# Kernel tuning notes

Hardware: AMD Instinct MI355X
Metric: run time of the kernel (lower is better)

## Reference

```python
import jax, jax.numpy as jnp
import numpy as np

N = 100000
E = 1600000
IN_C = 128
HID = 64
OUT_C = 112


def setup_inputs() -> dict:
    key = jax.random.key(0)
    ks = jax.random.split(key, 10)
    x = jax.random.normal(ks[0], (N, IN_C), dtype=jnp.float32)
    edge_index = jax.random.randint(ks[1], (2, E), 0, N, dtype=jnp.int32)
    s1 = 1.0 / np.sqrt(IN_C)
    s2 = 1.0 / np.sqrt(HID)
    return {
        "x": x,
        "edge_index": edge_index,
        "W1l": jax.random.uniform(ks[2], (IN_C, HID), jnp.float32, -s1, s1),
        "b1": jnp.zeros((HID,), jnp.float32),
        "W1r": jax.random.uniform(ks[3], (IN_C, HID), jnp.float32, -s1, s1),
        "W2l": jax.random.uniform(ks[4], (HID, HID), jnp.float32, -s2, s2),
        "b2": jnp.zeros((HID,), jnp.float32),
        "W2r": jax.random.uniform(ks[5], (HID, HID), jnp.float32, -s2, s2),
        "Wo": jax.random.uniform(ks[6], (HID, OUT_C), jnp.float32, -s2, s2),
        "bo": jnp.zeros((OUT_C,), jnp.float32),
    }


def _sage_conv(x, src, dst, Wl, b, Wr):
    # mean-aggregate neighbor messages (src -> dst), then linear + root linear
    msg = x[src]                                             # [E, F] gather
    agg = jax.ops.segment_sum(msg, dst, num_segments=N)      # [N, F] scatter-add
    deg = jax.ops.segment_sum(jnp.ones((src.shape[0],), x.dtype), dst, num_segments=N)
    mean = agg / jnp.maximum(deg, 1.0)[:, None]
    return mean @ Wl + b + x @ Wr


def reference(x, edge_index, W1l, b1, W1r, W2l, b2, W2r, Wo, bo):
    src, dst = edge_index[0], edge_index[1]
    h = jax.nn.relu(_sage_conv(x, src, dst, W1l, b1, W1r))
    # dropout disabled (inference / eval mode)
    h = jax.nn.relu(_sage_conv(h, src, dst, W2l, b2, W2r))
    return h @ Wo + bo
```

## Files before the change

### kernel.cpp

```cpp
#include <hip/hip_runtime.h>

typedef float f32x4 __attribute__((ext_vector_type(4)));
typedef short s16x8 __attribute__((ext_vector_type(8)));
typedef short s16x4 __attribute__((ext_vector_type(4)));

__device__ __forceinline__ unsigned short f2bf(float f) {
    unsigned u = __builtin_bit_cast(unsigned, f);
    unsigned r = (u + 0x7FFFu + ((u >> 16) & 1u)) >> 16;
    return (unsigned short)r;
}
__device__ __forceinline__ float bf2f(unsigned short h) {
    unsigned u = ((unsigned)h) << 16;
    return __builtin_bit_cast(float, u);
}
__device__ __forceinline__ float bflo(unsigned u) {
    return __builtin_bit_cast(float, u << 16);
}
__device__ __forceinline__ float bfhi(unsigned u) {
    return __builtin_bit_cast(float, u & 0xffff0000u);
}

__global__ __launch_bounds__(256)
void pack_frags(const float* __restrict__ W1l, const float* __restrict__ W1r,
                const float* __restrict__ W2l, const float* __restrict__ W2r,
                const float* __restrict__ Wo,
                short* __restrict__ PH1, short* __restrict__ PL1,
                short* __restrict__ PH2, short* __restrict__ PL2,
                short* __restrict__ PHo, short* __restrict__ PLo)
{
    const int tot = 2048 + 1024 + 896;
    for (int e = blockIdx.x * 256 + threadIdx.x; e < tot; e += gridDim.x * 256) {
        int lane, f, k0, c, stride;
        const float* W;
        short *PH, *PL;
        int idx;
        if (e < 2048) {
            idx = e; lane = e & 63; f = e >> 6;
            int kt = f & 3, ct = (f >> 2) & 3, m = f >> 4;
            W = m ? W1r : W1l; PH = PH1; PL = PL1;
            k0 = kt * 32 + ((lane >> 4) << 3);
            c  = ct * 16 + (lane & 15);
            stride = 64;
        } else if (e < 3072) {
            int e2 = e - 2048;
            idx = e2; lane = e2 & 63; f = e2 >> 6;
            int kt = f & 1, ct = (f >> 1) & 3, m = f >> 3;
            W = m ? W2r : W2l; PH = PH2; PL = PL2;
            k0 = kt * 32 + ((lane >> 4) << 3);
            c  = ct * 16 + (lane & 15);
            stride = 64;
        } else {
            int eo = e - 3072;
            idx = eo; lane = eo & 63; f = eo >> 6;
            int kt = f & 1, ct = f >> 1;
            W = Wo; PH = PHo; PL = PLo;
            k0 = kt * 32 + ((lane >> 4) << 3);
            c  = ct * 16 + (lane & 15);
            stride = 112;
        }
        short h[8], l[8];
        #pragma unroll
        for (int j = 0; j < 8; ++j) {
            float v = W[(size_t)(k0 + j) * stride + c];
            unsigned short hb = f2bf(v);
            h[j] = (short)hb;
            l[j] = (short)f2bf(v - bf2f(hb));
        }
        #pragma unroll
        for (int j = 0; j < 8; ++j) { PH[idx * 8 + j] = h[j]; PL[idx * 8 + j] = l[j]; }
    }
}

__global__ __launch_bounds__(512)
void fused_gemm1_count(const float* __restrict__ X, const short* __restrict__ PH,
                       const short* __restrict__ PL, unsigned short* __restrict__ Yl,
                       unsigned short* __restrict__ Yr, int n,
                       const int* __restrict__ dst, int* __restrict__ gcount,
                       int E, int B, int gemmBlocks)
{
    __shared__ unsigned short sT[8][16 * 72];
    __shared__ int lh[512];

    if ((int)blockIdx.x >= gemmBlocks) {
        for (int i = threadIdx.x; i < B; i += 512) lh[i] = 0;
        __syncthreads();
        long base = (long)(blockIdx.x - gemmBlocks) * 8192;
        #pragma unroll
        for (int j = 0; j < 16; ++j) {
            long e = base + j * 512 + threadIdx.x;
            if (e < E) atomicAdd(&lh[dst[e] >> 9], 1);
        }
        __syncthreads();
        for (int i = threadIdx.x; i < B; i += 512) {
            int v = lh[i];
            if (v) atomicAdd(&gcount[i], v);
        }
        return;
    }

    constexpr int K = 128, NKT = 4;
    const int lane = threadIdx.x & 63;
    const int wid  = threadIdx.x >> 6;
    const long ntile = ((long)n + 15) >> 4;
    long t = (long)blockIdx.x * 8 + wid;
    if (t >= ntile) return;
    const long rbase = t << 4;
    long arow = rbase + (lane & 15);
    if (arow >= n) arow = n - 1;
    const int koff = (lane >> 4) << 3;
    const float* xr = X + arow * K + koff;

    s16x8 Bh[NKT], Bl[NKT];
    #pragma unroll
    for (int kt = 0; kt < NKT; ++kt) {
        f32x4 a0 = *(const f32x4*)(xr + kt * 32);
        f32x4 a1 = *(const f32x4*)(xr + kt * 32 + 4);
        s16x8 h, l;
        #pragma unroll
        for (int j = 0; j < 4; ++j) {
            float v = a0[j]; unsigned short hb = f2bf(v);
            h[j] = (short)hb; l[j] = (short)f2bf(v - bf2f(hb));
            float v2 = a1[j]; unsigned short hb2 = f2bf(v2);
            h[4 + j] = (short)hb2; l[4 + j] = (short)f2bf(v2 - bf2f(hb2));
        }
        Bh[kt] = h; Bl[kt] = l;
    }

    f32x4 acc[2][4];
    #pragma unroll
    for (int m = 0; m < 2; ++m)
        #pragma unroll
        for (int ct = 0; ct < 4; ++ct) acc[m][ct] = (f32x4)(0.f);

    #pragma unroll
    for (int m = 0; m < 2; ++m)
    #pragma unroll
    for (int ct = 0; ct < 4; ++ct)
    #pragma unroll
    for (int kt = 0; kt < NKT; ++kt) {
        const int fidx = ((((m << 2) | ct) * NKT) + kt) * 64 + lane;
        s16x8 Ah = *(const s16x8*)(PH + (size_t)fidx * 8);
        s16x8 Al = *(const s16x8*)(PL + (size_t)fidx * 8);
        acc[m][ct] = __builtin_amdgcn_mfma_f32_16x16x32_bf16(Ah, Bh[kt], acc[m][ct], 0, 0, 0);
        acc[m][ct] = __builtin_amdgcn_mfma_f32_16x16x32_bf16(Al, Bh[kt], acc[m][ct], 0, 0, 0);
        acc[m][ct] = __builtin_amdgcn_mfma_f32_16x16x32_bf16(Ah, Bl[kt], acc[m][ct], 0, 0, 0);
    }

    const int wrow = lane & 15, q4 = (lane >> 4) << 2;
    #pragma unroll
    for (int m = 0; m < 2; ++m) {
        unsigned short* __restrict__ Y = m ? Yr : Yl;
        #pragma unroll
        for (int ct = 0; ct < 4; ++ct) {
            s16x4 pv;
            #pragma unroll
            for (int j = 0; j < 4; ++j) pv[j] = (short)f2bf(acc[m][ct][j]);
            *(s16x4*)&sT[wid][wrow * 72 + ct * 16 + q4] = pv;
        }
        asm volatile("s_waitcnt lgkmcnt(0)" ::: "memory");
        if (rbase + 16 <= (long)n) {
            #pragma unroll
            for (int s = 0; s < 2; ++s) {
                int f = s * 64 + lane;
                s16x8 v = *(const s16x8*)&sT[wid][(f >> 3) * 72 + ((f & 7) << 3)];
                *(s16x8*)&Y[rbase * 64 + (size_t)f * 8] = v;
            }
        } else {
            #pragma unroll
            for (int s = 0; s < 2; ++s) {
                int f = s * 64 + lane;
                s16x8 v = *(const s16x8*)&sT[wid][(f >> 3) * 72 + ((f & 7) << 3)];
                long g = rbase * 64 + (size_t)f * 8;
                #pragma unroll
                for (int jj = 0; jj < 8; ++jj)
                    if (g + jj < (long)n * 64) Y[g + jj] = (unsigned short)v[jj];
            }
        }
        asm volatile("s_waitcnt lgkmcnt(0)" ::: "memory");
    }
}


__global__ void bucket_scan(const int* __restrict__ gcount, int* __restrict__ gbase,
                            int* __restrict__ gcursor, int B, int E)
{
    __shared__ int s[256];
    int t = threadIdx.x;
    int v = (t < B) ? gcount[t] : 0;
    s[t] = v;
    __syncthreads();
    for (int off = 1; off < 256; off <<= 1) {
        int u = (t >= off) ? s[t - off] : 0;
        __syncthreads();
        s[t] += u;
        __syncthreads();
    }
    int ex = s[t] - v;
    if (t < B) { gbase[t] = ex; gcursor[t] = ex; }
    if (t == 0) gbase[B] = E;
}

__global__ __launch_bounds__(256)
void bucket_scatter(const int* __restrict__ src, const int* __restrict__ dst,
                    int* __restrict__ gcursor, int* __restrict__ packed, int E, int B)
{
    __shared__ int lh[256];
    __shared__ int lbase[256];
    for (int i = threadIdx.x; i < B; i += 256) lh[i] = 0;
    __syncthreads();
    long base = (long)blockIdx.x * 4096;
    int bkt[16], rnk[16], pk[16];
    #pragma unroll
    for (int j = 0; j < 16; ++j) {
        long e = base + j * 256 + threadIdx.x;
        if (e < E) {
            int d = dst[e], s = src[e];
            bkt[j] = d >> 9;
            pk[j]  = (s << 9) | (d & 511);
            rnk[j] = atomicAdd(&lh[bkt[j]], 1);
        } else bkt[j] = -1;
    }
    __syncthreads();
    for (int i = threadIdx.x; i < B; i += 256) {
        int v = lh[i];
        lbase[i] = v ? atomicAdd(&gcursor[i], v) : 0;
    }
    __syncthreads();
    #pragma unroll
    for (int j = 0; j < 16; ++j)
        if (bkt[j] >= 0) packed[lbase[bkt[j]] + rnk[j]] = pk[j];
}

__global__ __launch_bounds__(256)
void bucket_hist(const int* __restrict__ packed, const int* __restrict__ gbase,
                 int* __restrict__ degi, int n)
{
    __shared__ int h[512];
    int b = blockIdx.x, nb = b << 9;
    int cnt = n - nb; if (cnt > 512) cnt = 512;
    for (int i = threadIdx.x; i < 512; i += 256) h[i] = 0;
    __syncthreads();
    int s = gbase[b], e = gbase[b + 1];
    for (int i = s + threadIdx.x; i < e; i += 256)
        atomicAdd(&h[packed[i] & 511], 1);
    __syncthreads();
    for (int i = threadIdx.x; i < cnt; i += 256) degi[nb + i] = h[i];
}

__global__ __launch_bounds__(256)
void scan_chunk(const int* __restrict__ degi, int* __restrict__ rowptrP,
                int* __restrict__ partial, int n)
{
    __shared__ int s[256];
    const int b = blockIdx.x, t = threadIdx.x;
    const int base = b * 1024 + t * 4;
    int v[4], sum = 0;
    #pragma unroll
    for (int j = 0; j < 4; ++j) {
        int idx = base + j;
        v[j] = (idx < n) ? ((degi[idx] + 7) & ~7) : 0;
        sum += v[j];
    }
    s[t] = sum;
    __syncthreads();
    #pragma unroll
    for (int off = 1; off < 256; off <<= 1) {
        int x = (t >= off) ? s[t - off] : 0;
        __syncthreads();
        s[t] += x;
        __syncthreads();
    }
    int run = s[t] - sum;
    if (t == 255) partial[b] = s[255];
    #pragma unroll
    for (int j = 0; j < 4; ++j) {
        int idx = base + j;
        if (idx < n) { rowptrP[idx] = run; run += v[j]; }
    }
}

__global__ void scan_partials(int* partial, int nchunk)
{
    int t = threadIdx.x;
    if (nchunk > 128) {
        if (t == 0) {
            int acc = 0;
            for (int i = 0; i < nchunk; ++i) { int p = partial[i]; partial[i] = acc; acc += p; }
            partial[128] = acc;
        }
        return;
    }
    int a = (t < nchunk) ? partial[t] : 0;
    int b = (t + 64 < nchunk) ? partial[t + 64] : 0;
    int a0 = a, b0 = b;
    #pragma unroll
    for (int off = 1; off < 64; off <<= 1) {
        int u = __shfl_up(a, off, 64);
        if (t >= off) a += u;
    }
    int atot = __shfl(a, 63, 64);
    #pragma unroll
    for (int off = 1; off < 64; off <<= 1) {
        int u = __shfl_up(b, off, 64);
        if (t >= off) b += u;
    }
    int btot = __shfl(b, 63, 64);
    if (t < nchunk) partial[t] = a - a0;
    if (t + 64 < nchunk) partial[t + 64] = atot + b - b0;
    if (t == 0) partial[128] = atot + btot;
}

__global__ __launch_bounds__(256)
void finalize_rowptr(int* __restrict__ rowptrP, const int* __restrict__ partial,
                     unsigned* __restrict__ Adummy, int n)
{
    int i = blockIdx.x * blockDim.x + threadIdx.x;
    if (i < n) rowptrP[i] += partial[i >> 10];
    if (i == n) rowptrP[n] = partial[128];
    if (i < 32) Adummy[i] = 0u;
}

__global__ __launch_bounds__(256)
void bucket_fill(const int* __restrict__ packed, const int* __restrict__ gbase,
                 const int* __restrict__ rowptrP, int* __restrict__ csr,
                 int n, int dummyOff)
{
    __shared__ int cur[512];
    int b = blockIdx.x, nb = b << 9;
    int cnt = n - nb; if (cnt > 512) cnt = 512;
    for (int i = threadIdx.x; i < cnt; i += 256) cur[i] = rowptrP[nb + i];
    __syncthreads();
    int s = gbase[b], e = gbase[b + 1];
    for (int i = s + threadIdx.x; i < e; i += 256) {
        int p = packed[i];
        int pos = atomicAdd(&cur[p & 511], 1);
        csr[pos] = (p >> 9) << 7;
    }
    __syncthreads();
    for (int i = threadIdx.x; i < cnt; i += 256) {
        int end = rowptrP[nb + i + 1];
        for (int p = cur[i]; p < end; ++p) csr[p] = dummyOff;
    }
}

__global__ __launch_bounds__(256)
void pull_agg_pad(const unsigned short* __restrict__ feat, const int* __restrict__ rowptrP,
                  const int* __restrict__ degi, const int* __restrict__ csrB,
                  const unsigned short* __restrict__ C, const float* __restrict__ bias,
                  unsigned short* __restrict__ H, int n)
{
    const int lane = threadIdx.x & 63;
    const int half = lane >> 5;
    const int c    = lane & 31;
    const int wid  = threadIdx.x >> 6;
    const char* fb = (const char*)feat;
    const int cb   = c << 2;
    const float2 bv = *(const float2*)&bias[c * 2];

    const long w  = (long)blockIdx.x * 4 + wid;
    const long nw = (long)gridDim.x * 4;
    for (long rp = w * 2; rp < n; rp += nw * 2) {
        int2 rr = *(const int2*)&rowptrP[rp];
        int eB = (rp + 1 < n) ? rowptrP[rp + 2] : rr.y;

        const long r = rp + half;
        int dg = 1; unsigned cu = 0;
        if (r < n) {
            dg = degi[r];
            cu = *(const unsigned*)&C[(size_t)r * 64 + (c << 1)];
        }

        int iA = rr.x + (half << 2);
        int iB = rr.y + (half << 2);
        const int endA = rr.y, endB = eB;
        bool dA = iA < endA, dB = iB < endB;
        int4 oA = (int4)(0), oB = (int4)(0);
        if (dA) oA = *(const int4*)&csrB[iA];
        if (dB) oB = *(const int4*)&csrB[iB];

        float a0A = 0.f, a1A = 0.f, a0B = 0.f, a1B = 0.f;
        while (dA | dB) {
            unsigned uA0, uA1, uA2, uA3, uB0, uB1, uB2, uB3;
            if (dA) {
                uA0 = *(const unsigned*)(fb + oA.x + cb);
                uA1 = *(const unsigned*)(fb + oA.y + cb);
                uA2 = *(const unsigned*)(fb + oA.z + cb);
                uA3 = *(const unsigned*)(fb + oA.w + cb);
            }
            if (dB) {
                uB0 = *(const unsigned*)(fb + oB.x + cb);
                uB1 = *(const unsigned*)(fb + oB.y + cb);
                uB2 = *(const unsigned*)(fb + oB.z + cb);
                uB3 = *(const unsigned*)(fb + oB.w + cb);
            }
            int niA = iA + 8, niB = iB + 8;
            bool ndA = niA < endA, ndB = niB < endB;
            int4 tA = oA, tB = oB;
            if (ndA) tA = *(const int4*)&csrB[niA];
            if (ndB) tB = *(const int4*)&csrB[niB];
            if (dA) {
                a0A += bflo(uA0); a1A += bfhi(uA0);
                a0A += bflo(uA1); a1A += bfhi(uA1);
                a0A += bflo(uA2); a1A += bfhi(uA2);
                a0A += bflo(uA3); a1A += bfhi(uA3);
            }
            if (dB) {
                a0B += bflo(uB0); a1B += bfhi(uB0);
                a0B += bflo(uB1); a1B += bfhi(uB1);
                a0B += bflo(uB2); a1B += bfhi(uB2);
                a0B += bflo(uB3); a1B += bfhi(uB3);
            }
            oA = tA; oB = tB; iA = niA; iB = niB; dA = ndA; dB = ndB;
        }

        a0A += __shfl_xor(a0A, 32, 64);
        a1A += __shfl_xor(a1A, 32, 64);
        a0B += __shfl_xor(a0B, 32, 64);
        a1B += __shfl_xor(a1B, 32, 64);

        if (r < n) {
            float m0 = half ? a0B : a0A;
            float m1 = half ? a1B : a1A;
            float d = (float)dg;
            d = d > 1.f ? d : 1.f;
            float inv = 1.f / d;
            float v0 = m0 * inv + bflo(cu) + bv.x;
            float v1 = m1 * inv + bfhi(cu) + bv.y;
            v0 = v0 > 0.f ? v0 : 0.f;
            v1 = v1 > 0.f ? v1 : 0.f;
            unsigned pv = (unsigned)f2bf(v0) | ((unsigned)f2bf(v1) << 16);
            *(unsigned*)&H[(size_t)r * 64 + (c << 1)] = pv;
        }
    }
}


__global__ __launch_bounds__(512)
void dual_gemm_b16in(const unsigned short* __restrict__ X, const short* __restrict__ PH,
                     const short* __restrict__ PL, unsigned short* __restrict__ Yl,
                     unsigned short* __restrict__ Yr, int n)
{
    constexpr int NKT = 2;
    __shared__ unsigned short sT[8][16 * 72];
    const int lane = threadIdx.x & 63;
    const int wid  = threadIdx.x >> 6;
    const long ntile = ((long)n + 15) >> 4;
    long t = (long)blockIdx.x * 8 + wid;
    if (t >= ntile) return;
    const long rbase = t << 4;
    long arow = rbase + (lane & 15);
    if (arow >= n) arow = n - 1;
    const int koff = (lane >> 4) << 3;
    const unsigned short* xr = X + arow * 64 + koff;

    s16x8 Bv[NKT];
    #pragma unroll
    for (int kt = 0; kt < NKT; ++kt) Bv[kt] = *(const s16x8*)(xr + kt * 32);

    f32x4 acc[2][4];
    #pragma unroll
    for (int m = 0; m < 2; ++m)
        #pragma unroll
        for (int ct = 0; ct < 4; ++ct) acc[m][ct] = (f32x4)(0.f);

    #pragma unroll
    for (int m = 0; m < 2; ++m)
    #pragma unroll
    for (int ct = 0; ct < 4; ++ct)
    #pragma unroll
    for (int kt = 0; kt < NKT; ++kt) {
        const int fidx = ((((m << 2) | ct) * NKT) + kt) * 64 + lane;
        s16x8 Ah = *(const s16x8*)(PH + (size_t)fidx * 8);
        s16x8 Al = *(const s16x8*)(PL + (size_t)fidx * 8);
        acc[m][ct] = __builtin_amdgcn_mfma_f32_16x16x32_bf16(Ah, Bv[kt], acc[m][ct], 0, 0, 0);
        acc[m][ct] = __builtin_amdgcn_mfma_f32_16x16x32_bf16(Al, Bv[kt], acc[m][ct], 0, 0, 0);
    }

    const int wrow = lane & 15, q4 = (lane >> 4) << 2;
    #pragma unroll
    for (int m = 0; m < 2; ++m) {
        unsigned short* __restrict__ Y = m ? Yr : Yl;
        #pragma unroll
        for (int ct = 0; ct < 4; ++ct) {
            s16x4 pv;
            #pragma unroll
            for (int j = 0; j < 4; ++j) pv[j] = (short)f2bf(acc[m][ct][j]);
            *(s16x4*)&sT[wid][wrow * 72 + ct * 16 + q4] = pv;
        }
        asm volatile("s_waitcnt lgkmcnt(0)" ::: "memory");
        if (rbase + 16 <= (long)n) {
            #pragma unroll
            for (int s = 0; s < 2; ++s) {
                int f = s * 64 + lane;
                s16x8 v = *(const s16x8*)&sT[wid][(f >> 3) * 72 + ((f & 7) << 3)];
                *(s16x8*)&Y[rbase * 64 + (size_t)f * 8] = v;
            }
        } else {
            #pragma unroll
            for (int s = 0; s < 2; ++s) {
                int f = s * 64 + lane;
                s16x8 v = *(const s16x8*)&sT[wid][(f >> 3) * 72 + ((f & 7) << 3)];
                long g = rbase * 64 + (size_t)f * 8;
                #pragma unroll
                for (int jj = 0; jj < 8; ++jj)
                    if (g + jj < (long)n * 64) Y[g + jj] = (unsigned short)v[jj];
            }
        }
        asm volatile("s_waitcnt lgkmcnt(0)" ::: "memory");
    }
}

__global__ __launch_bounds__(512)
void gemm_out_mfma(const unsigned short* __restrict__ X, const short* __restrict__ PH,
                   const short* __restrict__ PL, const float* __restrict__ bo,
                   float* __restrict__ Y, int n)
{
    constexpr int NCT = 7;
    __shared__ float sT[8][16 * 120];
    const int lane = threadIdx.x & 63;
    const int wid  = threadIdx.x >> 6;
    const long ntile = ((long)n + 15) >> 4;
    long t = (long)blockIdx.x * 8 + wid;
    if (t >= ntile) return;
    const long rbase = t << 4;
    long arow = rbase + (lane & 15);
    if (arow >= n) arow = n - 1;
    const int koff = (lane >> 4) << 3;
    const unsigned short* xr = X + arow * 64 + koff;

    s16x8 Bv[2];
    #pragma unroll
    for (int kt = 0; kt < 2; ++kt) Bv[kt] = *(const s16x8*)(xr + kt * 32);

    f32x4 acc[NCT];
    #pragma unroll
    for (int ct = 0; ct < NCT; ++ct) acc[ct] = (f32x4)(0.f);

    #pragma unroll
    for (int ct = 0; ct < NCT; ++ct)
    #pragma unroll
    for (int kt = 0; kt < 2; ++kt) {
        const int fidx = (ct * 2 + kt) * 64 + lane;
        s16x8 Ah = *(const s16x8*)(PH + (size_t)fidx * 8);
        s16x8 Al = *(const s16x8*)(PL + (size_t)fidx * 8);
        acc[ct] = __builtin_amdgcn_mfma_f32_16x16x32_bf16(Ah, Bv[kt], acc[ct], 0, 0, 0);
        acc[ct] = __builtin_amdgcn_mfma_f32_16x16x32_bf16(Al, Bv[kt], acc[ct], 0, 0, 0);
    }

    const int wrow = lane & 15, q4 = (lane >> 4) << 2;
    #pragma unroll
    for (int ct = 0; ct < NCT; ++ct)
        *(f32x4*)&sT[wid][wrow * 120 + ct * 16 + q4] = acc[ct];
    asm volatile("s_waitcnt lgkmcnt(0)" ::: "memory");

    if (rbase + 16 <= (long)n) {
        #pragma unroll
        for (int s = 0; s < 7; ++s) {
            int f = s * 64 + lane;
            int row = f / 28, ch = f % 28;
            f32x4 v = *(const f32x4*)&sT[wid][row * 120 + ch * 4];
            f32x4 bv = *(const f32x4*)&bo[ch * 4];
            v.x += bv.x; v.y += bv.y; v.z += bv.z; v.w += bv.w;
            *(f32x4*)&Y[rbase * 112 + (size_t)f * 4] = v;
        }
    } else {
        #pragma unroll
        for (int s = 0; s < 7; ++s) {
            int f = s * 64 + lane;
            int row = f / 28, ch = f % 28;
            f32x4 v = *(const f32x4*)&sT[wid][row * 120 + ch * 4];
            #pragma unroll
            for (int jj = 0; jj < 4; ++jj) {
                long g = rbase * 112 + (size_t)f * 4 + jj;
                if (g < (long)n * 112) Y[g] = v[jj] + bo[ch * 4 + jj];
            }
        }
    }
}


extern "C" void kernel_launch(void* const* d_in, const int* in_sizes, int n_in,
                              void* d_out, int out_size, void* d_ws, size_t ws_size,
                              hipStream_t stream)
{
    const float* x   = (const float*)d_in[0];
    const int*   ei  = (const int*)d_in[1];
    const float* W1l = (const float*)d_in[2];
    const float* b1  = (const float*)d_in[3];
    const float* W1r = (const float*)d_in[4];
    const float* W2l = (const float*)d_in[5];
    const float* b2  = (const float*)d_in[6];
    const float* W2r = (const float*)d_in[7];
    const float* Wo  = (const float*)d_in[8];
    const float* bo  = (const float*)d_in[9];
    float* out = (float*)d_out;

    const int n = in_sizes[0] / 128;
    const int E = in_sizes[1] / 2;
    const int* srcI = ei;
    const int* dstI = ei + E;
    const int nchunk = (n + 1023) / 1024;
    const int nbkt   = (n + 511) >> 9;
    const size_t nn64 = (size_t)n * 64;
    const size_t csrCap = (size_t)E + (size_t)8 * n + 16;

    unsigned short* A = (unsigned short*)d_ws;
    unsigned short* C = A + nn64 + 64;
    unsigned short* H = C + nn64;
    int*   rowptrP= (int*)(H + nn64);
    int*   degi   = rowptrP + n + 1;
    int*   partial= degi + n;
    int*   csr    = partial + 130;
    int*   packed = csr + csrCap;
    int*   gcount = packed + E;
    int*   gbase  = gcount + nbkt;
    int*   gcursor= gbase + nbkt + 1;
    short* PH1    = (short*)(gcursor + nbkt);
    short* PL1    = PH1 + 16384;
    short* PH2    = PL1 + 16384;
    short* PL2    = PH2 + 8192;
    short* PHo    = PL2 + 8192;
    short* PLo    = PHo + 7168;

    const long ntile = ((long)n + 15) >> 4;
    const int gmf = (int)((ntile + 7) / 8);
    const int cntBlocks = (int)((E + 8191) / 8192);

    hipMemsetAsync(gcount, 0, (size_t)nbkt * sizeof(int), stream);
    pack_frags<<<16, 256, 0, stream>>>(W1l, W1r, W2l, W2r, Wo, PH1, PL1, PH2, PL2, PHo, PLo);

    fused_gemm1_count<<<gmf + cntBlocks, 512, 0, stream>>>(
        x, PH1, PL1, A, C, n, dstI, gcount, E, nbkt, gmf);

    bucket_scan<<<1, 256, 0, stream>>>(gcount, gbase, gcursor, nbkt, E);
    bucket_scatter<<<(int)((E + 4095) / 4096), 256, 0, stream>>>(srcI, dstI, gcursor, packed, E, nbkt);
    bucket_hist<<<nbkt, 256, 0, stream>>>(packed, gbase, degi, n);
    scan_chunk<<<nchunk, 256, 0, stream>>>(degi, rowptrP, partial, n);
    scan_partials<<<1, 64, 0, stream>>>(partial, nchunk);
    finalize_rowptr<<<(n + 256) / 256, 256, 0, stream>>>(rowptrP, partial,
                                                         (unsigned*)(A + nn64), n);
    bucket_fill<<<nbkt, 256, 0, stream>>>(packed, gbase, rowptrP, csr, n, n << 7);

    pull_agg_pad<<<4096, 256, 0, stream>>>(A, rowptrP, degi, csr, C, b1, H, n);

    dual_gemm_b16in<<<gmf, 512, 0, stream>>>(H, PH2, PL2, A, C, n);
    pull_agg_pad<<<4096, 256, 0, stream>>>(A, rowptrP, degi, csr, C, b2, H, n);

    gemm_out_mfma<<<gmf, 512, 0, stream>>>(H, PHo, PLo, bo, out, n);
}
```

Measured before the change: 212.4 us.

## Fuse neighbor aggregation with following GEMMs via per-wave LDS tiles

The pull-aggregation kernel now writes each 16-row tile of hidden activations into LDS and immediately runs the layer-2 dual GEMM (and, for the second layer, the output GEMM) on it. This removes the H round trip through global memory and two kernel launches. Separate A/C buffers are used per layer to avoid read/write hazards. The gcount memset is folded into pack_frags. In exchange, the grid becomes one wave per 16-row tile instead of a grid-stride loop, which may change load balance and latency hiding for the irregular gather.

After: 247.8 us. 1.17x slower.

```diff
diff --git a/kernel.cpp b/kernel.cpp
--- a/kernel.cpp
+++ b/kernel.cpp
@@ -26,8 +26,11 @@
                 const float* __restrict__ Wo,
                 short* __restrict__ PH1, short* __restrict__ PL1,
                 short* __restrict__ PH2, short* __restrict__ PL2,
-                short* __restrict__ PHo, short* __restrict__ PLo)
-{
+                short* __restrict__ PHo, short* __restrict__ PLo,
+                int* __restrict__ gcount, int nbkt)
+{
+    if (blockIdx.x == 0)
+        for (int i = threadIdx.x; i < nbkt; i += 256) gcount[i] = 0;
     const int tot = 2048 + 1024 + 896;
     for (int e = blockIdx.x * 256 + threadIdx.x; e < tot; e += gridDim.x * 256) {
         int lane, f, k0, c, stride;
@@ -312,12 +315,12 @@
 
 __global__ __launch_bounds__(256)
 void finalize_rowptr(int* __restrict__ rowptrP, const int* __restrict__ partial,
-                     unsigned* __restrict__ Adummy, int n)
+                     unsigned* __restrict__ A1dummy, unsigned* __restrict__ A2dummy, int n)
 {
     int i = blockIdx.x * blockDim.x + threadIdx.x;
     if (i < n) rowptrP[i] += partial[i >> 10];
     if (i == n) rowptrP[n] = partial[128];
-    if (i < 32) Adummy[i] = 0u;
+    if (i < 32) { A1dummy[i] = 0u; A2dummy[i] = 0u; }
 }
 
 __global__ __launch_bounds__(256)
@@ -344,11 +347,13 @@
 }
 
 __global__ __launch_bounds__(256)
-void pull_agg_pad(const unsigned short* __restrict__ feat, const int* __restrict__ rowptrP,
-                  const int* __restrict__ degi, const int* __restrict__ csrB,
-                  const unsigned short* __restrict__ C, const float* __restrict__ bias,
-                  unsigned short* __restrict__ H, int n)
-{
+void pull_gemm2(const unsigned short* __restrict__ feat, const int* __restrict__ rowptrP,
+                const int* __restrict__ degi, const int* __restrict__ csrB,
+                const unsigned short* __restrict__ C, const float* __restrict__ bias,
+                const short* __restrict__ PH, const short* __restrict__ PL,
+                unsigned short* __restrict__ Yl, unsigned short* __restrict__ Yr, int n)
+{
+    __shared__ unsigned short sT[4][16 * 72];
     const int lane = threadIdx.x & 63;
     const int half = lane >> 5;
     const int c    = lane & 31;
@@ -357,9 +362,15 @@
     const int cb   = c << 2;
     const float2 bv = *(const float2*)&bias[c * 2];
 
-    const long w  = (long)blockIdx.x * 4 + wid;
-    const long nw = (long)gridDim.x * 4;
-    for (long rp = w * 2; rp < n; rp += nw * 2) {
+    const long ntile = ((long)n + 15) >> 4;
+    const long t = (long)blockIdx.x * 4 + wid;
+    if (t >= ntile) return;
+    const long rbase = t << 4;
+
+    #pragma unroll 1
+    for (int pr = 0; pr < 8; ++pr) {
+        long rp = rbase + pr * 2;
+        if (rp >= n) break;
         int2 rr = *(const int2*)&rowptrP[rp];
         int eB = (rp + 1 < n) ? rowptrP[rp + 2] : rr.y;
 
@@ -429,33 +440,16 @@
             v0 = v0 > 0.f ? v0 : 0.f;
             v1 = v1 > 0.f ? v1 : 0.f;
             unsigned pv = (unsigned)f2bf(v0) | ((unsigned)f2bf(v1) << 16);
-            *(unsigned*)&H[(size_t)r * 64 + (c << 1)] = pv;
-        }
-    }
-}
-
-
-__global__ __launch_bounds__(512)
-void dual_gemm_b16in(const unsigned short* __restrict__ X, const short* __restrict__ PH,
-                     const short* __restrict__ PL, unsigned short* __restrict__ Yl,
-                     unsigned short* __restrict__ Yr, int n)
-{
-    constexpr int NKT = 2;
-    __shared__ unsigned short sT[8][16 * 72];
-    const int lane = threadIdx.x & 63;
-    const int wid  = threadIdx.x >> 6;
-    const long ntile = ((long)n + 15) >> 4;
-    long t = (long)blockIdx.x * 8 + wid;
-    if (t >= ntile) return;
-    const long rbase = t << 4;
-    long arow = rbase + (lane & 15);
-    if (arow >= n) arow = n - 1;
+            *(unsigned*)&sT[wid][(pr * 2 + half) * 72 + (c << 1)] = pv;
+        }
+    }
+    asm volatile("s_waitcnt lgkmcnt(0)" ::: "memory");
+
     const int koff = (lane >> 4) << 3;
-    const unsigned short* xr = X + arow * 64 + koff;
-
-    s16x8 Bv[NKT];
-    #pragma unroll
-    for (int kt = 0; kt < NKT; ++kt) Bv[kt] = *(const s16x8*)(xr + kt * 32);
+    s16x8 Bv[2];
+    #pragma unroll
+    for (int kt = 0; kt < 2; ++kt)
+        Bv[kt] = *(const s16x8*)&sT[wid][(lane & 15) * 72 + kt * 32 + koff];
 
     f32x4 acc[2][4];
     #pragma unroll
@@ -468,8 +462,8 @@
     #pragma unroll
     for (int ct = 0; ct < 4; ++ct)
     #pragma unroll
-    for (int kt = 0; kt < NKT; ++kt) {
-        const int fidx = ((((m << 2) | ct) * NKT) + kt) * 64 + lane;
+    for (int kt = 0; kt < 2; ++kt) {
+        const int fidx = ((((m << 2) | ct) * 2) + kt) * 64 + lane;
         s16x8 Ah = *(const s16x8*)(PH + (size_t)fidx * 8);
         s16x8 Al = *(const s16x8*)(PL + (size_t)fidx * 8);
         acc[m][ct] = __builtin_amdgcn_mfma_f32_16x16x32_bf16(Ah, Bv[kt], acc[m][ct], 0, 0, 0);
@@ -510,27 +504,112 @@
     }
 }
 
-__global__ __launch_bounds__(512)
-void gemm_out_mfma(const unsigned short* __restrict__ X, const short* __restrict__ PH,
-                   const short* __restrict__ PL, const float* __restrict__ bo,
-                   float* __restrict__ Y, int n)
+__global__ __launch_bounds__(256)
+void pull_out(const unsigned short* __restrict__ feat, const int* __restrict__ rowptrP,
+              const int* __restrict__ degi, const int* __restrict__ csrB,
+              const unsigned short* __restrict__ C, const float* __restrict__ bias,
+              const short* __restrict__ PH, const short* __restrict__ PL,
+              const float* __restrict__ bo, float* __restrict__ Y, int n)
 {
     constexpr int NCT = 7;
-    __shared__ float sT[8][16 * 120];
+    __shared__ float sO[4][16 * 120];
     const int lane = threadIdx.x & 63;
+    const int half = lane >> 5;
+    const int c    = lane & 31;
     const int wid  = threadIdx.x >> 6;
+    const char* fb = (const char*)feat;
+    const int cb   = c << 2;
+    const float2 bv = *(const float2*)&bias[c * 2];
+    unsigned short* sI = (unsigned short*)&sO[wid][0];
+
     const long ntile = ((long)n + 15) >> 4;
-    long t = (long)blockIdx.x * 8 + wid;
+    const long t = (long)blockIdx.x * 4 + wid;
     if (t >= ntile) return;
     const long rbase = t << 4;
-    long arow = rbase + (lane & 15);
-    if (arow >= n) arow = n - 1;
+
+    #pragma unroll 1
+    for (int pr = 0; pr < 8; ++pr) {
+        long rp = rbase + pr * 2;
+        if (rp >= n) break;
+        int2 rr = *(const int2*)&rowptrP[rp];
+        int eB = (rp + 1 < n) ? rowptrP[rp + 2] : rr.y;
+
+        const long r = rp + half;
+        int dg = 1; unsigned cu = 0;
+        if (r < n) {
+            dg = degi[r];
+            cu = *(const unsigned*)&C[(size_t)r * 64 + (c << 1)];
+        }
+
+        int iA = rr.x + (half << 2);
+        int iB = rr.y + (half << 2);
+        const int endA = rr.y, endB = eB;
+        bool dA = iA < endA, dB = iB < endB;
+        int4 oA = (int4)(0), oB = (int4)(0);
+        if (dA) oA = *(const int4*)&csrB[iA];
+        if (dB) oB = *(const int4*)&csrB[iB];
+
+        float a0A = 0.f, a1A = 0.f, a0B = 0.f, a1B = 0.f;
+        while (dA | dB) {
+            unsigned uA0, uA1, uA2, uA3, uB0, uB1, uB2, uB3;
+            if (dA) {
+                uA0 = *(const unsigned*)(fb + oA.x + cb);
+                uA1 = *(const unsigned*)(fb + oA.y + cb);
+                uA2 = *(const unsigned*)(fb + oA.z + cb);
+                uA3 = *(const unsigned*)(fb + oA.w + cb);
+            }
+            if (dB) {
+                uB0 = *(const unsigned*)(fb + oB.x + cb);
+                uB1 = *(const unsigned*)(fb + oB.y + cb);
+                uB2 = *(const unsigned*)(fb + oB.z + cb);
+                uB3 = *(const unsigned*)(fb + oB.w + cb);
+            }
+            int niA = iA + 8, niB = iB + 8;
+            bool ndA = niA < endA, ndB = niB < endB;
+            int4 tA = oA, tB = oB;
+            if (ndA) tA = *(const int4*)&csrB[niA];
+            if (ndB) tB = *(const int4*)&csrB[niB];
+            if (dA) {
+                a0A += bflo(uA0); a1A += bfhi(uA0);
+                a0A += bflo(uA1); a1A += bfhi(uA1);
+                a0A += bflo(uA2); a1A += bfhi(uA2);
+                a0A += bflo(uA3); a1A += bfhi(uA3);
+            }
+            if (dB) {
+                a0B += bflo(uB0); a1B += bfhi(uB0);
+                a0B += bflo(uB1); a1B += bfhi(uB1);
+                a0B += bflo(uB2); a1B += bfhi(uB2);
+                a0B += bflo(uB3); a1B += bfhi(uB3);
+            }
+            oA = tA; oB = tB; iA = niA; iB = niB; dA = ndA; dB = ndB;
+        }
+
+        a0A += __shfl_xor(a0A, 32, 64);
+        a1A += __shfl_xor(a1A, 32, 64);
+        a0B += __shfl_xor(a0B, 32, 64);
+        a1B += __shfl_xor(a1B, 32, 64);
+
+        if (r < n) {
+            float m0 = half ? a0B : a0A;
+            float m1 = half ? a1B : a1A;
+            float d = (float)dg;
+            d = d > 1.f ? d : 1.f;
+            float inv = 1.f / d;
+            float v0 = m0 * inv + bflo(cu) + bv.x;
+            float v1 = m1 * inv + bfhi(cu) + bv.y;
+            v0 = v0 > 0.f ? v0 : 0.f;
+            v1 = v1 > 0.f ? v1 : 0.f;
+            unsigned pv = (unsigned)f2bf(v0) | ((unsigned)f2bf(v1) << 16);
+            *(unsigned*)&sI[(pr * 2 + half) * 72 + (c << 1)] = pv;
+        }
+    }
+    asm volatile("s_waitcnt lgkmcnt(0)" ::: "memory");
+
     const int koff = (lane >> 4) << 3;
-    const unsigned short* xr = X + arow * 64 + koff;
-
     s16x8 Bv[2];
     #pragma unroll
-    for (int kt = 0; kt < 2; ++kt) Bv[kt] = *(const s16x8*)(xr + kt * 32);
+    for (int kt = 0; kt < 2; ++kt)
+        Bv[kt] = *(const s16x8*)&sI[(lane & 15) * 72 + kt * 32 + koff];
 
     f32x4 acc[NCT];
     #pragma unroll
@@ -550,7 +629,7 @@
     const int wrow = lane & 15, q4 = (lane >> 4) << 2;
     #pragma unroll
     for (int ct = 0; ct < NCT; ++ct)
-        *(f32x4*)&sT[wid][wrow * 120 + ct * 16 + q4] = acc[ct];
+        *(f32x4*)&sO[wid][wrow * 120 + ct * 16 + q4] = acc[ct];
     asm volatile("s_waitcnt lgkmcnt(0)" ::: "memory");
 
     if (rbase + 16 <= (long)n) {
@@ -558,9 +637,9 @@
         for (int s = 0; s < 7; ++s) {
             int f = s * 64 + lane;
             int row = f / 28, ch = f % 28;
-            f32x4 v = *(const f32x4*)&sT[wid][row * 120 + ch * 4];
-            f32x4 bv = *(const f32x4*)&bo[ch * 4];
-            v.x += bv.x; v.y += bv.y; v.z += bv.z; v.w += bv.w;
+            f32x4 v = *(const f32x4*)&sO[wid][row * 120 + ch * 4];
+            f32x4 b4 = *(const f32x4*)&bo[ch * 4];
+            v.x += b4.x; v.y += b4.y; v.z += b4.z; v.w += b4.w;
             *(f32x4*)&Y[rbase * 112 + (size_t)f * 4] = v;
         }
     } else {
@@ -568,7 +647,7 @@
         for (int s = 0; s < 7; ++s) {
             int f = s * 64 + lane;
             int row = f / 28, ch = f % 28;
-            f32x4 v = *(const f32x4*)&sT[wid][row * 120 + ch * 4];
+            f32x4 v = *(const f32x4*)&sO[wid][row * 120 + ch * 4];
             #pragma unroll
             for (int jj = 0; jj < 4; ++jj) {
                 long g = rbase * 112 + (size_t)f * 4 + jj;
@@ -604,10 +683,11 @@
     const size_t nn64 = (size_t)n * 64;
     const size_t csrCap = (size_t)E + (size_t)8 * n + 16;
 
-    unsigned short* A = (unsigned short*)d_ws;
-    unsigned short* C = A + nn64 + 64;
-    unsigned short* H = C + nn64;
-    int*   rowptrP= (int*)(H + nn64);
+    unsigned short* A1 = (unsigned short*)d_ws;
+    unsigned short* C1 = A1 + nn64 + 64;
+    unsigned short* A2 = C1 + nn64;
+    unsigned short* C2 = A2 + nn64 + 64;
+    int*   rowptrP= (int*)(C2 + nn64);
     int*   degi   = rowptrP + n + 1;
     int*   partial= degi + n;
     int*   csr    = partial + 130;
@@ -624,13 +704,14 @@
 
     const long ntile = ((long)n + 15) >> 4;
     const int gmf = (int)((ntile + 7) / 8);
+    const int gpf = (int)((ntile + 3) / 4);
     const int cntBlocks = (int)((E + 8191) / 8192);
 
-    hipMemsetAsync(gcount, 0, (size_t)nbkt * sizeof(int), stream);
-    pack_frags<<<16, 256, 0, stream>>>(W1l, W1r, W2l, W2r, Wo, PH1, PL1, PH2, PL2, PHo, PLo);
+    pack_frags<<<16, 256, 0, stream>>>(W1l, W1r, W2l, W2r, Wo,
+                                       PH1, PL1, PH2, PL2, PHo, PLo, gcount, nbkt);
 
     fused_gemm1_count<<<gmf + cntBlocks, 512, 0, stream>>>(
-        x, PH1, PL1, A, C, n, dstI, gcount, E, nbkt, gmf);
+        x, PH1, PL1, A1, C1, n, dstI, gcount, E, nbkt, gmf);
 
     bucket_scan<<<1, 256, 0, stream>>>(gcount, gbase, gcursor, nbkt, E);
     bucket_scatter<<<(int)((E + 4095) / 4096), 256, 0, stream>>>(srcI, dstI, gcursor, packed, E, nbkt);
@@ -638,13 +719,13 @@
     scan_chunk<<<nchunk, 256, 0, stream>>>(degi, rowptrP, partial, n);
     scan_partials<<<1, 64, 0, stream>>>(partial, nchunk);
     finalize_rowptr<<<(n + 256) / 256, 256, 0, stream>>>(rowptrP, partial,
-                                                         (unsigned*)(A + nn64), n);
+                                                         (unsigned*)(A1 + nn64),
+                                                         (unsigned*)(A2 + nn64), n);
     bucket_fill<<<nbkt, 256, 0, stream>>>(packed, gbase, rowptrP, csr, n, n << 7);
 
-    pull_agg_pad<<<4096, 256, 0, stream>>>(A, rowptrP, degi, csr, C, b1, H, n);
-
-    dual_gemm_b16in<<<gmf, 512, 0, stream>>>(H, PH2, PL2, A, C, n);
-    pull_agg_pad<<<4096, 256, 0, stream>>>(A, rowptrP, degi, csr, C, b2, H, n);
-
-    gemm_out_mfma<<<gmf, 512, 0, stream>>>(H, PHo, PLo, bo, out, n);
-}
+    pull_gemm2<<<gpf, 256, 0, stream>>>(A1, rowptrP, degi, csr, C1, b1,
+                                        PH2, PL2, A2, C2, n);
+
+    pull_out<<<gpf, 256, 0, stream>>>(A2, rowptrP, degi, csr, C2, b2,
+                                      PHo, PLo, bo, out, n);
+}
```

## Fuse histogram with row scan, pad CSR rows to 16, widen gather

Applied to the files above, without the earlier changes.

Merges the per-bucket degree histogram with the row-pointer scan so each bucket block scans its own 512 rows, and folds the gcount memset into pack_frags, removing two launches. CSR rows are now padded to multiples of 16 instead of 8, letting the pull aggregation issue 8 feature gathers per half-wave per iteration instead of 4 for more memory-level parallelism. The cost is more padding edges, which means extra dummy gathers and a larger CSR buffer. The partials scan is rewritten for up to 256 buckets.

New measurement: 216.9 us. 1.02x slower.

```diff
diff --git a/kernel.cpp b/kernel.cpp
--- a/kernel.cpp
+++ b/kernel.cpp
@@ -26,8 +26,11 @@
                 const float* __restrict__ Wo,
                 short* __restrict__ PH1, short* __restrict__ PL1,
                 short* __restrict__ PH2, short* __restrict__ PL2,
-                short* __restrict__ PHo, short* __restrict__ PLo)
-{
+                short* __restrict__ PHo, short* __restrict__ PLo,
+                int* __restrict__ gcount, int nbkt)
+{
+    if (blockIdx.x == 0)
+        for (int i = threadIdx.x; i < nbkt; i += 256) gcount[i] = 0;
     const int tot = 2048 + 1024 + 896;
     for (int e = blockIdx.x * 256 + threadIdx.x; e < tot; e += gridDim.x * 256) {
         int lane, f, k0, c, stride;
@@ -232,91 +235,63 @@
 }
 
 __global__ __launch_bounds__(256)
-void bucket_hist(const int* __restrict__ packed, const int* __restrict__ gbase,
-                 int* __restrict__ degi, int n)
+void hist_scan(const int* __restrict__ packed, const int* __restrict__ gbase,
+               int* __restrict__ degi, int* __restrict__ rowptrP,
+               int* __restrict__ partial, int n)
 {
     __shared__ int h[512];
-    int b = blockIdx.x, nb = b << 9;
+    __shared__ int s[256];
+    const int b = blockIdx.x, t = threadIdx.x, nb = b << 9;
     int cnt = n - nb; if (cnt > 512) cnt = 512;
-    for (int i = threadIdx.x; i < 512; i += 256) h[i] = 0;
-    __syncthreads();
-    int s = gbase[b], e = gbase[b + 1];
-    for (int i = s + threadIdx.x; i < e; i += 256)
+    for (int i = t; i < 512; i += 256) h[i] = 0;
+    __syncthreads();
+    int bs = gbase[b], be = gbase[b + 1];
+    for (int i = bs + t; i < be; i += 256)
         atomicAdd(&h[packed[i] & 511], 1);
     __syncthreads();
-    for (int i = threadIdx.x; i < cnt; i += 256) degi[nb + i] = h[i];
-}
-
-__global__ __launch_bounds__(256)
-void scan_chunk(const int* __restrict__ degi, int* __restrict__ rowptrP,
-                int* __restrict__ partial, int n)
+    int e0 = (2 * t     < cnt) ? h[2 * t]     : 0;
+    int e1 = (2 * t + 1 < cnt) ? h[2 * t + 1] : 0;
+    int p0 = (e0 + 15) & ~15;
+    int p1 = (e1 + 15) & ~15;
+    int mysum = p0 + p1;
+    s[t] = mysum;
+    __syncthreads();
+    for (int off = 1; off < 256; off <<= 1) {
+        int u = (t >= off) ? s[t - off] : 0;
+        __syncthreads();
+        s[t] += u;
+        __syncthreads();
+    }
+    int excl = s[t] - mysum;
+    if (2 * t < cnt)     { degi[nb + 2 * t]     = e0; rowptrP[nb + 2 * t]     = excl; }
+    if (2 * t + 1 < cnt) { degi[nb + 2 * t + 1] = e1; rowptrP[nb + 2 * t + 1] = excl + p0; }
+    if (t == 255) partial[b] = s[255];
+}
+
+__global__ void scan_partials(int* __restrict__ partial, int B)
 {
     __shared__ int s[256];
-    const int b = blockIdx.x, t = threadIdx.x;
-    const int base = b * 1024 + t * 4;
-    int v[4], sum = 0;
-    #pragma unroll
-    for (int j = 0; j < 4; ++j) {
-        int idx = base + j;
-        v[j] = (idx < n) ? ((degi[idx] + 7) & ~7) : 0;
-        sum += v[j];
-    }
-    s[t] = sum;
-    __syncthreads();
-    #pragma unroll
+    int t = threadIdx.x;
+    int v = (t < B) ? partial[t] : 0;
+    s[t] = v;
+    __syncthreads();
     for (int off = 1; off < 256; off <<= 1) {
-        int x = (t >= off) ? s[t - off] : 0;
-        __syncthreads();
-        s[t] += x;
-        __syncthreads();
-    }
-    int run = s[t] - sum;
-    if (t == 255) partial[b] = s[255];
-    #pragma unroll
-    for (int j = 0; j < 4; ++j) {
-        int idx = base + j;
-        if (idx < n) { rowptrP[idx] = run; run += v[j]; }
-    }
-}
-
-__global__ void scan_partials(int* partial, int nchunk)
-{
-    int t = threadIdx.x;
-    if (nchunk > 128) {
-        if (t == 0) {
-            int acc = 0;
-            for (int i = 0; i < nchunk; ++i) { int p = partial[i]; partial[i] = acc; acc += p; }
-            partial[128] = acc;
-        }
-        return;
-    }
-    int a = (t < nchunk) ? partial[t] : 0;
-    int b = (t + 64 < nchunk) ? partial[t + 64] : 0;
-    int a0 = a, b0 = b;
-    #pragma unroll
-    for (int off = 1; off < 64; off <<= 1) {
-        int u = __shfl_up(a, off, 64);
-        if (t >= off) a += u;
-    }
-    int atot = __shfl(a, 63, 64);
-    #pragma unroll
-    for (int off = 1; off < 64; off <<= 1) {
-        int u = __shfl_up(b, off, 64);
-        if (t >= off) b += u;
-    }
-    int btot = __shfl(b, 63, 64);
-    if (t < nchunk) partial[t] = a - a0;
-    if (t + 64 < nchunk) partial[t + 64] = atot + b - b0;
-    if (t == 0) partial[128] = atot + btot;
+        int u = (t >= off) ? s[t - off] : 0;
+        __syncthreads();
+        s[t] += u;
+        __syncthreads();
+    }
+    if (t < B) partial[t] = s[t] - v;
+    if (t == 255) partial[B] = s[255];
 }
 
 __global__ __launch_bounds__(256)
 void finalize_rowptr(int* __restrict__ rowptrP, const int* __restrict__ partial,
-                     unsigned* __restrict__ Adummy, int n)
+                     unsigned* __restrict__ Adummy, int n, int nbkt)
 {
     int i = blockIdx.x * blockDim.x + threadIdx.x;
-    if (i < n) rowptrP[i] += partial[i >> 10];
-    if (i == n) rowptrP[n] = partial[128];
+    if (i < n) rowptrP[i] += partial[i >> 9];
+    if (i == n) rowptrP[n] = partial[nbkt];
     if (i < 32) Adummy[i] = 0u;
 }
 
@@ -355,6 +330,7 @@
     const int wid  = threadIdx.x >> 6;
     const char* fb = (const char*)feat;
     const int cb   = c << 2;
+    const int ho   = half << 2;
     const float2 bv = *(const float2*)&bias[c * 2];
 
     const long w  = (long)blockIdx.x * 4 + wid;
@@ -370,47 +346,49 @@
             cu = *(const unsigned*)&C[(size_t)r * 64 + (c << 1)];
         }
 
-        int iA = rr.x + (half << 2);
-        int iB = rr.y + (half << 2);
+        int iA = rr.x, iB = rr.y;
         const int endA = rr.y, endB = eB;
         bool dA = iA < endA, dB = iB < endB;
-        int4 oA = (int4)(0), oB = (int4)(0);
-        if (dA) oA = *(const int4*)&csrB[iA];
-        if (dB) oB = *(const int4*)&csrB[iB];
+        int4 oA0 = (int4)(0), oA1 = (int4)(0), oB0 = (int4)(0), oB1 = (int4)(0);
+        if (dA) { oA0 = *(const int4*)&csrB[iA + ho]; oA1 = *(const int4*)&csrB[iA + 8 + ho]; }
+        if (dB) { oB0 = *(const int4*)&csrB[iB + ho]; oB1 = *(const int4*)&csrB[iB + 8 + ho]; }
 
         float a0A = 0.f, a1A = 0.f, a0B = 0.f, a1B = 0.f;
         while (dA | dB) {
-            unsigned uA0, uA1, uA2, uA3, uB0, uB1, uB2, uB3;
+            unsigned uA[8], uB[8];
             if (dA) {
-                uA0 = *(const unsigned*)(fb + oA.x + cb);
-                uA1 = *(const unsigned*)(fb + oA.y + cb);
-                uA2 = *(const unsigned*)(fb + oA.z + cb);
-                uA3 = *(const unsigned*)(fb + oA.w + cb);
+                uA[0] = *(const unsigned*)(fb + oA0.x + cb);
+                uA[1] = *(const unsigned*)(fb + oA0.y + cb);
+                uA[2] = *(const unsigned*)(fb + oA0.z + cb);
+                uA[3] = *(const unsigned*)(fb + oA0.w + cb);
+                uA[4] = *(const unsigned*)(fb + oA1.x + cb);
+                uA[5] = *(const unsigned*)(fb + oA1.y + cb);
+                uA[6] = *(const unsigned*)(fb + oA1.z + cb);
+                uA[7] = *(const unsigned*)(fb + oA1.w + cb);
             }
             if (dB) {
-                uB0 = *(const unsigned*)(fb + oB.x + cb);
-                uB1 = *(const unsigned*)(fb + oB.y + cb);
-                uB2 = *(const unsigned*)(fb + oB.z + cb);
-                uB3 = *(const unsigned*)(fb + oB.w + cb);
-            }
-            int niA = iA + 8, niB = iB + 8;
+                uB[0] = *(const unsigned*)(fb + oB0.x + cb);
+                uB[1] = *(const unsigned*)(fb + oB0.y + cb);
+                uB[2] = *(const unsigned*)(fb + oB0.z + cb);
+                uB[3] = *(const unsigned*)(fb + oB0.w + cb);
+                uB[4] = *(const unsigned*)(fb + oB1.x + cb);
+                uB[5] = *(const unsigned*)(fb + oB1.y + cb);
+                uB[6] = *(const unsigned*)(fb + oB1.z + cb);
+                uB[7] = *(const unsigned*)(fb + oB1.w + cb);
+            }
+            int niA = iA + 16, niB = iB + 16;
             bool ndA = niA < endA, ndB = niB < endB;
-            int4 tA = oA, tB = oB;
-            if (ndA) tA = *(const int4*)&csrB[niA];
-            if (ndB) tB = *(const int4*)&csrB[niB];
+            if (ndA) { oA0 = *(const int4*)&csrB[niA + ho]; oA1 = *(const int4*)&csrB[niA + 8 + ho]; }
+            if (ndB) { oB0 = *(const int4*)&csrB[niB + ho]; oB1 = *(const int4*)&csrB[niB + 8 + ho]; }
             if (dA) {
-                a0A += bflo(uA0); a1A += bfhi(uA0);
-                a0A += bflo(uA1); a1A += bfhi(uA1);
-                a0A += bflo(uA2); a1A += bfhi(uA2);
-                a0A += bflo(uA3); a1A += bfhi(uA3);
+                #pragma unroll
+                for (int j = 0; j < 8; ++j) { a0A += bflo(uA[j]); a1A += bfhi(uA[j]); }
             }
             if (dB) {
-                a0B += bflo(uB0); a1B += bfhi(uB0);
-                a0B += bflo(uB1); a1B += bfhi(uB1);
-                a0B += bflo(uB2); a1B += bfhi(uB2);
-                a0B += bflo(uB3); a1B += bfhi(uB3);
-            }
-            oA = tA; oB = tB; iA = niA; iB = niB; dA = ndA; dB = ndB;
+                #pragma unroll
+                for (int j = 0; j < 8; ++j) { a0B += bflo(uB[j]); a1B += bfhi(uB[j]); }
+            }
+            iA = niA; iB = niB; dA = ndA; dB = ndB;
         }
 
         a0A += __shfl_xor(a0A, 32, 64);
@@ -559,8 +537,8 @@
             int f = s * 64 + lane;
             int row = f / 28, ch = f % 28;
             f32x4 v = *(const f32x4*)&sT[wid][row * 120 + ch * 4];
-            f32x4 bv = *(const f32x4*)&bo[ch * 4];
-            v.x += bv.x; v.y += bv.y; v.z += bv.z; v.w += bv.w;
+            f32x4 b4 = *(const f32x4*)&bo[ch * 4];
+            v.x += b4.x; v.y += b4.y; v.z += b4.z; v.w += b4.w;
             *(f32x4*)&Y[rbase * 112 + (size_t)f * 4] = v;
         }
     } else {
@@ -599,10 +577,9 @@
     const int E = in_sizes[1] / 2;
     const int* srcI = ei;
     const int* dstI = ei + E;
-    const int nchunk = (n + 1023) / 1024;
     const int nbkt   = (n + 511) >> 9;
     const size_t nn64 = (size_t)n * 64;
-    const size_t csrCap = (size_t)E + (size_t)8 * n + 16;
+    const size_t csrCap = (size_t)E + (size_t)16 * n + 32;
 
     unsigned short* A = (unsigned short*)d_ws;
     unsigned short* C = A + nn64 + 64;
@@ -610,7 +587,7 @@
     int*   rowptrP= (int*)(H + nn64);
     int*   degi   = rowptrP + n + 1;
     int*   partial= degi + n;
-    int*   csr    = partial + 130;
+    int*   csr    = partial + 260;
     int*   packed = csr + csrCap;
     int*   gcount = packed + E;
     int*   gbase  = gcount + nbkt;
@@ -626,19 +603,18 @@
     const int gmf = (int)((ntile + 7) / 8);
     const int cntBlocks = (int)((E + 8191) / 8192);
 
-    hipMemsetAsync(gcount, 0, (size_t)nbkt * sizeof(int), stream);
-    pack_frags<<<16, 256, 0, stream>>>(W1l, W1r, W2l, W2r, Wo, PH1, PL1, PH2, PL2, PHo, PLo);
+    pack_frags<<<16, 256, 0, stream>>>(W1l, W1r, W2l, W2r, Wo,
+                                       PH1, PL1, PH2, PL2, PHo, PLo, gcount, nbkt);
 
     fused_gemm1_count<<<gmf + cntBlocks, 512, 0, stream>>>(
         x, PH1, PL1, A, C, n, dstI, gcount, E, nbkt, gmf);
 
     bucket_scan<<<1, 256, 0, stream>>>(gcount, gbase, gcursor, nbkt, E);
     bucket_scatter<<<(int)((E + 4095) / 4096), 256, 0, stream>>>(srcI, dstI, gcursor, packed, E, nbkt);
-    bucket_hist<<<nbkt, 256, 0, stream>>>(packed, gbase, degi, n);
-    scan_chunk<<<nchunk, 256, 0, stream>>>(degi, rowptrP, partial, n);
-    scan_partials<<<1, 64, 0, stream>>>(partial, nchunk);
+    hist_scan<<<nbkt, 256, 0, stream>>>(packed, gbase, degi, rowptrP, partial, n);
+    scan_partials<<<1, 256, 0, stream>>>(partial, nbkt);
     finalize_rowptr<<<(n + 256) / 256, 256, 0, stream>>>(rowptrP, partial,
-                                                         (unsigned*)(A + nn64), n);
+                                                         (unsigned*)(A + nn64), n, nbkt);
     bucket_fill<<<nbkt, 256, 0, stream>>>(packed, gbase, rowptrP, csr, n, n << 7);
 
     pull_agg_pad<<<4096, 256, 0, stream>>>(A, rowptrP, degi, csr, C, b1, H, n);
```
